# Optimization experiments

Hardware: AMD Instinct MI355X
Metric: run time of the kernel (lower is better)

The kernel has to match this reference:

```python
import jax, jax.numpy as jnp
import numpy as np
from jax import lax

V, D, L, H, MAXLEN = 32000, 512, 6, 8, 1024
DH = D // H
DFF = 4 * D
B, T = 8, 1024


def _ln(x, g, b, eps=1e-5):
    m = jnp.mean(x, axis=-1, keepdims=True)
    v = jnp.var(x, axis=-1, keepdims=True)
    return (x - m) * lax.rsqrt(v + eps) * g + b


def setup_inputs() -> dict:
    key = jax.random.key(0)
    ks = jax.random.split(key, 16)
    s = 0.02
    inp = {
        "idx": jax.random.randint(ks[0], (B, T), 0, V, dtype=jnp.int32),
        "wte": jax.random.normal(ks[1], (V, D), jnp.float32) * s,   # tied with head
        "wpe": jax.random.normal(ks[2], (MAXLEN, D), jnp.float32) * s,
        # per-layer stacked params [L, ...]
        "ln1_g": jnp.ones((L, D), jnp.float32),
        "ln1_b": jnp.zeros((L, D), jnp.float32),
        "w_qkv": jax.random.normal(ks[3], (L, D, 3 * D), jnp.float32) * s,
        "b_qkv": jnp.zeros((L, 3 * D), jnp.float32),
        "w_ao": jax.random.normal(ks[4], (L, D, D), jnp.float32) * s,
        "b_ao": jnp.zeros((L, D), jnp.float32),
        "ln2_g": jnp.ones((L, D), jnp.float32),
        "ln2_b": jnp.zeros((L, D), jnp.float32),
        "w_fc": jax.random.normal(ks[5], (L, D, DFF), jnp.float32) * s,
        "b_fc": jnp.zeros((L, DFF), jnp.float32),
        "w_pr": jax.random.normal(ks[6], (L, DFF, D), jnp.float32) * s,
        "b_pr": jnp.zeros((L, D), jnp.float32),
        "lnf_g": jnp.ones((D,), jnp.float32),
        "lnf_b": jnp.zeros((D,), jnp.float32),
    }
    return inp


def reference(idx, wte, wpe, ln1_g, ln1_b, w_qkv, b_qkv, w_ao, b_ao,
              ln2_g, ln2_b, w_fc, b_fc, w_pr, b_pr, lnf_g, lnf_b):
    Bx, Tx = idx.shape
    x = wte[idx] + wpe[:Tx]                      # [B,T,D]
    causal = jnp.tril(jnp.ones((Tx, Tx), bool))  # [T,T]
    scale = 1.0 / np.sqrt(DH)

    def block(x, p):
        (g1, b1, wqkv, bqkv, wao, bao, g2, b2, wfc, bfc, wpr, bpr) = p
        h = _ln(x, g1, b1)
        qkv = h @ wqkv + bqkv                    # [B,T,3D]
        q, k, v = jnp.split(qkv, 3, axis=-1)
        q = q.reshape(Bx, Tx, H, DH)
        k = k.reshape(Bx, Tx, H, DH)
        v = v.reshape(Bx, Tx, H, DH)
        att = jnp.einsum('bqhd,bkhd->bhqk', q, k) * scale
        att = jnp.where(causal, att, -jnp.inf)
        att = jax.nn.softmax(att, axis=-1)
        y = jnp.einsum('bhqk,bkhd->bqhd', att, v).reshape(Bx, Tx, D)
        x = x + y @ wao + bao
        h = _ln(x, g2, b2)
        h = jax.nn.gelu(h @ wfc + bfc, approximate=False)
        x = x + h @ wpr + bpr
        return x, None

    params = (ln1_g, ln1_b, w_qkv, b_qkv, w_ao, b_ao,
              ln2_g, ln2_b, w_fc, b_fc, w_pr, b_pr)
    x, _ = lax.scan(block, x, params)
    x = _ln(x, lnf_g, lnf_b)
    logits = x @ wte.T                           # tied head, [B,T,V]
    return logits
```

## Files before the change

### kernel.cpp

```cpp
#include <hip/hip_runtime.h>
#include <hip/hip_bf16.h>
#include <math.h>

#define V_   32000
#define D_   512
#define L_   6
#define H_   8
#define DH_  64
#define DFF_ 2048
#define B_   8
#define T_   1024
#define BT_  (B_*T_)

typedef __attribute__((ext_vector_type(4))) float f32x4;
typedef __attribute__((ext_vector_type(8))) short short8;
using bf16_t = __hip_bfloat16;

__device__ __forceinline__ float b2f(unsigned short u) {
    union { unsigned int i; float f; } v; v.i = ((unsigned int)u) << 16; return v.f;
}
__device__ __forceinline__ unsigned short f2b(float f) {
    bf16_t h = __float2bfloat16(f);
    return *reinterpret_cast<unsigned short*>(&h);
}
__device__ __forceinline__ void gl16(const void* g, void* l) {
    __builtin_amdgcn_global_load_lds((const __attribute__((address_space(1))) void*)g,
                                     (__attribute__((address_space(3))) void*)l, 16, 0, 0);
}
__device__ __forceinline__ float gelu_exact(float v) {
    return 0.5f * v * (1.0f + erff(v * 0.70710678118654752f));
}

__global__ __launch_bounds__(128) void embed_ln_kernel(
        const int* __restrict__ idx, const float* __restrict__ wte,
        const float* __restrict__ wpe, const float* __restrict__ g,
        const float* __restrict__ bb, float* __restrict__ x,
        bf16_t* __restrict__ hout) {
    int bt = blockIdx.x;
    int tt = bt & (T_ - 1);
    int tok = idx[bt];
    int i = threadIdx.x;
    float4 a = ((const float4*)(wte + (size_t)tok * D_))[i];
    float4 p = ((const float4*)(wpe + (size_t)tt * D_))[i];
    float4 v = make_float4(a.x + p.x, a.y + p.y, a.z + p.z, a.w + p.w);
    ((float4*)(x + (size_t)bt * D_))[i] = v;

    float s  = v.x + v.y + v.z + v.w;
    float sq = v.x*v.x + v.y*v.y + v.z*v.z + v.w*v.w;
    #pragma unroll
    for (int o = 32; o > 0; o >>= 1) {
        s  += __shfl_down(s,  o);
        sq += __shfl_down(sq, o);
    }
    __shared__ float ss[2], ssq[2];
    if ((i & 63) == 0) { ss[i >> 6] = s; ssq[i >> 6] = sq; }
    __syncthreads();
    float mean = (ss[0] + ss[1]) * (1.0f / D_);
    float var  = (ssq[0] + ssq[1]) * (1.0f / D_) - mean * mean;
    float rstd = rsqrtf(var + 1e-5f);
    float4 gg = ((const float4*)g)[i];
    float4 b2 = ((const float4*)bb)[i];
    ushort4 o4;
    o4.x = f2b((v.x - mean) * rstd * gg.x + b2.x);
    o4.y = f2b((v.y - mean) * rstd * gg.y + b2.y);
    o4.z = f2b((v.z - mean) * rstd * gg.z + b2.z);
    o4.w = f2b((v.w - mean) * rstd * gg.w + b2.w);
    ((ushort4*)(hout + (size_t)bt * D_))[i] = o4;
}

__global__ __launch_bounds__(128) void ln_kernel(
        const float* __restrict__ x, const float* __restrict__ g,
        const float* __restrict__ b, bf16_t* __restrict__ out) {
    int bt = blockIdx.x;
    int i  = threadIdx.x;
    float4 v = ((const float4*)(x + (size_t)bt * D_))[i];
    float s  = v.x + v.y + v.z + v.w;
    float sq = v.x*v.x + v.y*v.y + v.z*v.z + v.w*v.w;
    #pragma unroll
    for (int o = 32; o > 0; o >>= 1) {
        s  += __shfl_down(s,  o);
        sq += __shfl_down(sq, o);
    }
    __shared__ float ss[2], ssq[2];
    if ((i & 63) == 0) { ss[i >> 6] = s; ssq[i >> 6] = sq; }
    __syncthreads();
    float mean = (ss[0] + ss[1]) * (1.0f / D_);
    float var  = (ssq[0] + ssq[1]) * (1.0f / D_) - mean * mean;
    float rstd = rsqrtf(var + 1e-5f);
    float4 gg = ((const float4*)g)[i];
    float4 bb = ((const float4*)b)[i];
    ushort4 o4;
    o4.x = f2b((v.x - mean) * rstd * gg.x + bb.x);
    o4.y = f2b((v.y - mean) * rstd * gg.y + bb.y);
    o4.z = f2b((v.z - mean) * rstd * gg.z + bb.z);
    o4.w = f2b((v.w - mean) * rstd * gg.w + bb.w);
    ((ushort4*)(out + (size_t)bt * D_))[i] = o4;
}

__global__ __launch_bounds__(256) void conv_kernel(
        const float* __restrict__ s, bf16_t* __restrict__ d, int n4) {
    int i = blockIdx.x * 256 + threadIdx.x;
    if (i >= n4) return;
    float4 f = ((const float4*)s)[i];
    ushort4 u = make_ushort4(f2b(f.x), f2b(f.y), f2b(f.z), f2b(f.w));
    ((ushort4*)d)[i] = u;
}

__global__ __launch_bounds__(256) void tconv_kernel(
        const float* __restrict__ src, bf16_t* __restrict__ dst, int K, int N) {
    size_t ls = (size_t)K * N;
    const float* s = src + blockIdx.z * ls;
    bf16_t* d = dst + blockIdx.z * ls;
    __shared__ float tile[32][33];
    int n0 = blockIdx.x * 32, k0 = blockIdx.y * 32;
    int c = threadIdx.x & 31, r8 = threadIdx.x >> 5;
    #pragma unroll
    for (int i = 0; i < 4; ++i) {
        int r = r8 + i * 8;
        tile[r][c] = s[(size_t)(k0 + r) * N + n0 + c];
    }
    __syncthreads();
    #pragma unroll
    for (int i = 0; i < 4; ++i) {
        int r = r8 + i * 8;
        d[(size_t)(n0 + r) * K + k0 + c] = __float2bfloat16(tile[c][r]);
    }
}

template<int BK, int ACT, bool OBF, bool RES, bool CONVB>
__global__ __launch_bounds__(256) void mm_kernel(
        const bf16_t* __restrict__ A,
        const bf16_t* __restrict__ Bt,
        const float*  __restrict__ Bf,
        const float*  __restrict__ bias,
        const float*  __restrict__ res,
        void* __restrict__ Cout,
        int M, int N, int K)
{
    constexpr int SLOTS = BK / 8;
    constexpr int CH    = BK / 16;
    __shared__ __align__(16) unsigned short As[128 * BK];
    __shared__ __align__(16) unsigned short Bs[128 * BK];
    const int nwg = gridDim.x;
    const int orig = blockIdx.x;
    const int q8 = nwg >> 3, r8 = nwg & 7;
    const int xcd = orig & 7, lin = orig >> 3;
    const int wg = (xcd < r8) ? xcd * (q8 + 1) + lin
                              : r8 * (q8 + 1) + (xcd - r8) * q8 + lin;
    const int gym = M >> 7;
    const int by = wg % gym;
    const int bx = wg / gym;

    const int t    = threadIdx.x;
    const int row0 = by * 128;
    const int col0 = bx * 128;
    const int lane = t & 63;
    const int wid  = t >> 6;
    const int wm   = (wid & 1) * 64;
    const int wn   = (wid >> 1) * 64;
    const int fr   = lane & 15;
    const int fq   = lane >> 4;

    f32x4 acc[4][4];
    #pragma unroll
    for (int m = 0; m < 4; ++m)
        #pragma unroll
        for (int n = 0; n < 4; ++n)
            acc[m][n] = (f32x4)(0.0f);

    const unsigned short* Ab  = (const unsigned short*)A;
    const unsigned short* Btb = (const unsigned short*)Bt;

    for (int k0 = 0; k0 < K; k0 += BK) {
        __syncthreads();
        #pragma unroll
        for (int i = 0; i < CH; ++i) {
            int c = t + i * 256;
            int row = c / SLOTS;
            int sl  = (c & (SLOTS - 1)) ^ (row & 7);
            gl16(Ab + (size_t)(row0 + row) * K + k0 + sl * 8, As + (size_t)c * 8);
        }
        if (!CONVB) {
            #pragma unroll
            for (int i = 0; i < CH; ++i) {
                int c = t + i * 256;
                int row = c / SLOTS;
                int sl  = (c & (SLOTS - 1)) ^ (row & 7);
                gl16(Btb + (size_t)(col0 + row) * K + k0 + sl * 8, Bs + (size_t)c * 8);
            }
        } else {
            #pragma unroll
            for (int i = 0; i < CH; ++i) {
                int c = t + i * 256;
                int row = c / SLOTS;
                int sl  = (c & (SLOTS - 1)) ^ (row & 7);
                const float* sp = Bf + (size_t)(col0 + row) * K + k0 + sl * 8;
                float4 f0 = ((const float4*)sp)[0];
                float4 f1 = ((const float4*)sp)[1];
                short8 pk;
                pk[0] = f2b(f0.x); pk[1] = f2b(f0.y); pk[2] = f2b(f0.z); pk[3] = f2b(f0.w);
                pk[4] = f2b(f1.x); pk[5] = f2b(f1.y); pk[6] = f2b(f1.z); pk[7] = f2b(f1.w);
                *(short8*)(Bs + (size_t)c * 8) = pk;
            }
        }
        __syncthreads();

        #pragma unroll
        for (int kk = 0; kk < BK / 32; ++kk) {
            short8 av[4], bv[4];
            #pragma unroll
            for (int m = 0; m < 4; ++m) {
                int R = wm + m * 16 + fr;
                int sl = (kk * 4 + fq) ^ (fr & 7);
                av[m] = *(const short8*)(As + (size_t)R * BK + sl * 8);
            }
            #pragma unroll
            for (int n = 0; n < 4; ++n) {
                int R = wn + n * 16 + fr;
                int sl = (kk * 4 + fq) ^ (fr & 7);
                bv[n] = *(const short8*)(Bs + (size_t)R * BK + sl * 8);
            }
            #pragma unroll
            for (int m = 0; m < 4; ++m)
                #pragma unroll
                for (int n = 0; n < 4; ++n)
                    acc[m][n] = __builtin_amdgcn_mfma_f32_16x16x32_bf16(av[m], bv[n], acc[m][n], 0, 0, 0);
        }
    }

    #pragma unroll
    for (int n = 0; n < 4; ++n) {
        int col = col0 + wn + n * 16 + fr;
        float bb = bias ? bias[col] : 0.0f;
        #pragma unroll
        for (int m = 0; m < 4; ++m) {
            int rbase = row0 + wm + m * 16 + fq * 4;
            #pragma unroll
            for (int r = 0; r < 4; ++r) {
                float v = acc[m][n][r] + bb;
                if (ACT == 1) v = gelu_exact(v);
                size_t off = (size_t)(rbase + r) * N + col;
                if (RES) v += res[off];
                if (OBF) ((bf16_t*)Cout)[off] = __float2bfloat16(v);
                else     ((float*)Cout)[off]  = v;
            }
        }
    }
}

#define MM8_PHASE(MH, NH, HALF, SRCB, R0, DSTB)                               \
  {                                                                           \
    short8 af[2][4]; short8 bg[2][2];                                         \
    _Pragma("unroll")                                                         \
    for (int ks = 0; ks < 2; ++ks) {                                          \
      _Pragma("unroll")                                                       \
      for (int m = 0; m < 4; ++m) {                                           \
        int row = ((MH)*4 + m)*32 + wm*16 + fr;                               \
        int sl  = (ks*4 + fq) ^ (fr & 7);                                     \
        af[ks][m] = *(const short8*)(curA + (size_t)row*64 + (size_t)sl*8);   \
      }                                                                       \
      _Pragma("unroll")                                                       \
      for (int n = 0; n < 2; ++n) {                                           \
        int col = ((NH)*2 + n)*64 + wn*16 + fr;                               \
        int sl  = (ks*4 + fq) ^ (fr & 7);                                     \
        bg[ks][n] = *(const short8*)(curB + (size_t)col*64 + (size_t)sl*8);   \
      }                                                                       \
    }                                                                         \
    if (pf) {                                                                 \
      _Pragma("unroll")                                                       \
      for (int i = 0; i < 2; ++i) {                                           \
        int c = (HALF)*1024 + i*512 + t;                                      \
        int row = c >> 3, sl = (c & 7) ^ (row & 7);                           \
        gl16(SRCB + (size_t)((R0) + row)*K + k0n + sl*8,                      \
             DSTB + (size_t)c*8);                                             \
      }                                                                       \
      asm volatile("s_waitcnt vmcnt(2)" ::: "memory");                        \
    } else if ((MH) == 0 && (NH) == 0) {                                      \
      asm volatile("s_waitcnt vmcnt(0)" ::: "memory");                        \
    }                                                                         \
    asm volatile("s_barrier" ::: "memory");                                   \
    asm volatile("s_waitcnt lgkmcnt(0)" ::: "memory");                        \
    __builtin_amdgcn_sched_barrier(0);                                        \
    __builtin_amdgcn_s_setprio(1);                                            \
    _Pragma("unroll")                                                         \
    for (int ks = 0; ks < 2; ++ks)                                            \
      _Pragma("unroll")                                                       \
      for (int m = 0; m < 4; ++m)                                             \
        _Pragma("unroll")                                                     \
        for (int n = 0; n < 2; ++n)                                           \
          acc[(MH)*4+m][(NH)*2+n] = __builtin_amdgcn_mfma_f32_16x16x32_bf16(  \
              af[ks][m], bg[ks][n], acc[(MH)*4+m][(NH)*2+n], 0, 0, 0);        \
    __builtin_amdgcn_s_setprio(0);                                            \
    __builtin_amdgcn_sched_barrier(0);                                        \
    asm volatile("s_barrier" ::: "memory");                                   \
  }

template<int ACT, bool OBF>
__global__ __launch_bounds__(512) void mm8_kernel(
        const bf16_t* __restrict__ A,
        const bf16_t* __restrict__ Bt,
        const float*  __restrict__ bias,
        void* __restrict__ Cout,
        int M, int N, int K)
{
    __shared__ __align__(16) unsigned short sA[2][256 * 64];
    __shared__ __align__(16) unsigned short sB[2][256 * 64];

    const int nwg = gridDim.x;
    const int orig = blockIdx.x;
    const int q8 = nwg >> 3, r8 = nwg & 7;
    const int xcd = orig & 7, lin = orig >> 3;
    const int wg = (xcd < r8) ? xcd * (q8 + 1) + lin
                              : r8 * (q8 + 1) + (xcd - r8) * q8 + lin;
    const int gym = M >> 8;
    const int by = wg % gym;
    const int bx = wg / gym;
    const int row0 = by * 256;
    const int col0 = bx * 256;

    const int t    = threadIdx.x;
    const int lane = t & 63;
    const int wid  = t >> 6;
    const int wm   = wid >> 2;
    const int wn   = wid & 3;
    const int fr   = lane & 15;
    const int fq   = lane >> 4;

    const unsigned short* Ab = (const unsigned short*)A;
    const unsigned short* Bb = (const unsigned short*)Bt;

    f32x4 acc[8][4];
    #pragma unroll
    for (int m = 0; m < 8; ++m)
        #pragma unroll
        for (int n = 0; n < 4; ++n)
            acc[m][n] = (f32x4)(0.0f);

    const int NK = K >> 6;

    #pragma unroll
    for (int h = 0; h < 2; ++h)
        #pragma unroll
        for (int i = 0; i < 2; ++i) {
            int c = h * 1024 + i * 512 + t;
            int row = c >> 3, sl = (c & 7) ^ (row & 7);
            gl16(Ab + (size_t)(row0 + row) * K + sl * 8, &sA[0][(size_t)c * 8]);
            gl16(Bb + (size_t)(col0 + row) * K + sl * 8, &sB[0][(size_t)c * 8]);
        }
    asm volatile("s_waitcnt vmcnt(0)" ::: "memory");
    asm volatile("s_barrier" ::: "memory");

    for (int s = 0; s < NK; ++s) {
        const unsigned short* curA = sA[s & 1];
        const unsigned short* curB = sB[s & 1];
        unsigned short* nxA = (unsigned short*)sA[(s + 1) & 1];
        unsigned short* nxB = (unsigned short*)sB[(s + 1) & 1];
        const int k0n = (s + 1) << 6;
        const bool pf = (s + 1) < NK;
        MM8_PHASE(0, 0, 0, Ab, row0, nxA)
        MM8_PHASE(1, 0, 0, Bb, col0, nxB)
        MM8_PHASE(0, 1, 1, Ab, row0, nxA)
        MM8_PHASE(1, 1, 1, Bb, col0, nxB)
    }

    #pragma unroll
    for (int n = 0; n < 4; ++n) {
        int col = col0 + n * 64 + wn * 16 + fr;
        float bb = bias ? bias[col] : 0.0f;
        #pragma unroll
        for (int m = 0; m < 8; ++m) {
            int rbase = row0 + m * 32 + wm * 16 + fq * 4;
            #pragma unroll
            for (int r = 0; r < 4; ++r) {
                float v = acc[m][n][r] + bb;
                if (ACT == 1) v = gelu_exact(v);
                size_t off = (size_t)(rbase + r) * N + col;
                if (OBF) ((bf16_t*)Cout)[off] = __float2bfloat16(v);
                else     ((float*)Cout)[off]  = v;
            }
        }
    }
}

__global__ __launch_bounds__(512, 2) void flash_kernel(
        const bf16_t* __restrict__ qkv, bf16_t* __restrict__ y)
{
    __shared__ __align__(16) unsigned short Ks[2][64][72];
    __shared__ __align__(16) unsigned short Vt[2][64][72];
    __shared__ __align__(16) unsigned short Pls[128][72];

    const int qt = (T_ / 128 - 1) - (blockIdx.x >> 6);
    const int bh = blockIdx.x & 63;
    const int h  = bh & (H_ - 1);
    const int b  = bh >> 3;
    const int t  = threadIdx.x;
    const int lane = t & 63;
    const int w    = t >> 6;
    const int fr   = lane & 15;
    const int fq   = lane >> 4;
    const int sj   = t >> 3;
    const int sseg = t & 7;

    const unsigned short* qkvb = (const unsigned short*)qkv;

    short8 avq[2];
    {
        const unsigned short* qrow = qkvb +
            (size_t)(b * T_ + qt * 128 + w * 16 + fr) * (3 * D_) + h * DH_;
        avq[0] = *(const short8*)(qrow + fq * 8);
        avq[1] = *(const short8*)(qrow + 32 + fq * 8);
    }

    float mi[4], li[4];
    f32x4 oacc[4];
    #pragma unroll
    for (int r = 0; r < 4; ++r) { mi[r] = -INFINITY; li[r] = 0.0f; }
    #pragma unroll
    for (int d = 0; d < 4; ++d) oacc[d] = (f32x4)(0.0f);

    const int nt = 2 * qt + 2;

    short8 kreg, vreg;
    {
        const unsigned short* kr = qkvb +
            (size_t)(b * T_ + sj) * (3 * D_) + D_ + h * DH_ + sseg * 8;
        kreg = *(const short8*)kr;
        vreg = *(const short8*)(kr + D_);
    }
    *(short8*)&Ks[0][sj][sseg * 8] = kreg;
    {
        int dbase = sseg * 8;
        Vt[0][dbase + 0][sj] = vreg[0]; Vt[0][dbase + 1][sj] = vreg[1];
        Vt[0][dbase + 2][sj] = vreg[2]; Vt[0][dbase + 3][sj] = vreg[3];
        Vt[0][dbase + 4][sj] = vreg[4]; Vt[0][dbase + 5][sj] = vreg[5];
        Vt[0][dbase + 6][sj] = vreg[6]; Vt[0][dbase + 7][sj] = vreg[7];
    }
    __syncthreads();

    for (int jt = 0; jt < nt; ++jt) {
        const int cur = jt & 1;
        const bool pf = (jt + 1) < nt;
        if (pf) {
            const unsigned short* kr = qkvb +
                (size_t)(b * T_ + (jt + 1) * 64 + sj) * (3 * D_) + D_ + h * DH_ + sseg * 8;
            kreg = *(const short8*)kr;
            vreg = *(const short8*)(kr + D_);
        }

        f32x4 s[4];
        #pragma unroll
        for (int jb = 0; jb < 4; ++jb) s[jb] = (f32x4)(0.0f);
        #pragma unroll
        for (int ks = 0; ks < 2; ++ks) {
            #pragma unroll
            for (int jb = 0; jb < 4; ++jb) {
                short8 bv = *(const short8*)(&Ks[cur][jb * 16 + fr][ks * 32 + fq * 8]);
                s[jb] = __builtin_amdgcn_mfma_f32_16x16x32_bf16(avq[ks], bv, s[jb], 0, 0, 0);
            }
        }

        float sv[4][4];
        const int qgb = qt * 128 + w * 16 + fq * 4;
        #pragma unroll
        for (int jb = 0; jb < 4; ++jb) {
            int jg = jt * 64 + jb * 16 + fr;
            #pragma unroll
            for (int r = 0; r < 4; ++r) {
                float x = s[jb][r] * 0.125f;
                sv[jb][r] = (jg > qgb + r) ? -INFINITY : x;
            }
        }

        #pragma unroll
        for (int r = 0; r < 4; ++r) {
            float tm = fmaxf(fmaxf(sv[0][r], sv[1][r]), fmaxf(sv[2][r], sv[3][r]));
            tm = fmaxf(tm, __shfl_xor(tm, 1));
            tm = fmaxf(tm, __shfl_xor(tm, 2));
            tm = fmaxf(tm, __shfl_xor(tm, 4));
            tm = fmaxf(tm, __shfl_xor(tm, 8));
            float mnew = fmaxf(mi[r], tm);
            float corr = __expf(mi[r] - mnew);
            float tsum = 0.0f;
            #pragma unroll
            for (int jb = 0; jb < 4; ++jb) {
                float p = __expf(sv[jb][r] - mnew);
                sv[jb][r] = p;
                tsum += p;
            }
            tsum += __shfl_xor(tsum, 1);
            tsum += __shfl_xor(tsum, 2);
            tsum += __shfl_xor(tsum, 4);
            tsum += __shfl_xor(tsum, 8);
            li[r] = li[r] * corr + tsum;
            mi[r] = mnew;
            #pragma unroll
            for (int db = 0; db < 4; ++db) oacc[db][r] *= corr;
        }

        #pragma unroll
        for (int jb = 0; jb < 4; ++jb)
            #pragma unroll
            for (int r = 0; r < 4; ++r)
                Pls[w * 16 + fq * 4 + r][jb * 16 + fr] = f2b(sv[jb][r]);

        #pragma unroll
        for (int ks = 0; ks < 2; ++ks) {
            short8 ap = *(const short8*)(&Pls[w * 16 + fr][ks * 32 + fq * 8]);
            #pragma unroll
            for (int db = 0; db < 4; ++db) {
                short8 bv = *(const short8*)(&Vt[cur][db * 16 + fr][ks * 32 + fq * 8]);
                oacc[db] = __builtin_amdgcn_mfma_f32_16x16x32_bf16(ap, bv, oacc[db], 0, 0, 0);
            }
        }

        __syncthreads();
        if (pf) {
            *(short8*)&Ks[cur ^ 1][sj][sseg * 8] = kreg;
            int dbase = sseg * 8;
            Vt[cur ^ 1][dbase + 0][sj] = vreg[0]; Vt[cur ^ 1][dbase + 1][sj] = vreg[1];
            Vt[cur ^ 1][dbase + 2][sj] = vreg[2]; Vt[cur ^ 1][dbase + 3][sj] = vreg[3];
            Vt[cur ^ 1][dbase + 4][sj] = vreg[4]; Vt[cur ^ 1][dbase + 5][sj] = vreg[5];
            Vt[cur ^ 1][dbase + 6][sj] = vreg[6]; Vt[cur ^ 1][dbase + 7][sj] = vreg[7];
        }
        __syncthreads();
    }

    unsigned short* yb = (unsigned short*)y;
    #pragma unroll
    for (int r = 0; r < 4; ++r) {
        float inv = 1.0f / li[r];
        size_t row = (size_t)(b * T_ + qt * 128 + w * 16 + fq * 4 + r);
        #pragma unroll
        for (int db = 0; db < 4; ++db)
            yb[row * D_ + h * DH_ + db * 16 + fr] = f2b(oacc[db][r] * inv);
    }
}

extern "C" void kernel_launch(void* const* d_in, const int* in_sizes, int n_in,
                              void* d_out, int out_size, void* d_ws, size_t ws_size,
                              hipStream_t stream) {
    const int*   idx   = (const int*)  d_in[0];
    const float* wte   = (const float*)d_in[1];
    const float* wpe   = (const float*)d_in[2];
    const float* ln1_g = (const float*)d_in[3];
    const float* ln1_b = (const float*)d_in[4];
    const float* w_qkv = (const float*)d_in[5];
    const float* b_qkv = (const float*)d_in[6];
    const float* w_ao  = (const float*)d_in[7];
    const float* b_ao  = (const float*)d_in[8];
    const float* ln2_g = (const float*)d_in[9];
    const float* ln2_b = (const float*)d_in[10];
    const float* w_fc  = (const float*)d_in[11];
    const float* b_fc  = (const float*)d_in[12];
    const float* w_pr  = (const float*)d_in[13];
    const float* b_pr  = (const float*)d_in[14];
    const float* lnf_g = (const float*)d_in[15];
    const float* lnf_b = (const float*)d_in[16];
    float* outf = (float*)d_out;

    char* base = (char*)d_out;
    size_t off = 0;
    auto alloc = [&](size_t bytes) {
        void* p = base + off;
        off += (bytes + 255) & ~(size_t)255;
        return p;
    };
    bf16_t* wqkvT = (bf16_t*)alloc((size_t)L_ * 3 * D_ * D_ * 2);
    bf16_t* waoT  = (bf16_t*)alloc((size_t)L_ * D_ * D_ * 2);
    bf16_t* wfcT  = (bf16_t*)alloc((size_t)L_ * DFF_ * D_ * 2);
    bf16_t* wprT  = (bf16_t*)alloc((size_t)L_ * D_ * DFF_ * 2);
    bf16_t* qkvb  = (bf16_t*)alloc((size_t)BT_ * 3 * D_ * 2);
    bf16_t* yb    = (bf16_t*)alloc((size_t)BT_ * D_ * 2);
    bf16_t* hab   = (bf16_t*)alloc((size_t)BT_ * D_ * 2);
    bf16_t* fcb   = (bf16_t*)alloc((size_t)BT_ * DFF_ * 2);
    float*  xb    = (float*) alloc((size_t)BT_ * D_ * 4);

    bf16_t* hfin = (bf16_t*)d_ws;
    size_t hbytes = ((size_t)BT_ * D_ * 2 + 255) & ~(size_t)255;
    bool wte_ws = ws_size >= hbytes + (size_t)V_ * D_ * 2 + 256;
    bf16_t* wteb = wte_ws ? (bf16_t*)((char*)d_ws + hbytes) : nullptr;

    if (wte_ws)
        conv_kernel<<<(V_ * D_ / 4 + 255) / 256, 256, 0, stream>>>(wte, wteb, V_ * D_ / 4);
    tconv_kernel<<<dim3(3 * D_ / 32, D_ / 32, L_), 256, 0, stream>>>(w_qkv, wqkvT, D_, 3 * D_);
    tconv_kernel<<<dim3(D_ / 32, D_ / 32, L_), 256, 0, stream>>>(w_ao, waoT, D_, D_);
    tconv_kernel<<<dim3(DFF_ / 32, D_ / 32, L_), 256, 0, stream>>>(w_fc, wfcT, D_, DFF_);
    tconv_kernel<<<dim3(D_ / 32, DFF_ / 32, L_), 256, 0, stream>>>(w_pr, wprT, DFF_, D_);

    embed_ln_kernel<<<BT_, 128, 0, stream>>>(idx, wte, wpe, ln1_g, ln1_b, xb, hab);

    for (int l = 0; l < L_; ++l) {
        mm8_kernel<0, true><<<(BT_ / 256) * (3 * D_ / 256), 512, 0, stream>>>(
            hab, wqkvT + (size_t)l * 3 * D_ * D_, b_qkv + (size_t)l * 3 * D_,
            qkvb, BT_, 3 * D_, D_);
        flash_kernel<<<512, 512, 0, stream>>>(qkvb, yb);
        mm_kernel<128, 0, false, true, false><<<4 * 64, 256, 0, stream>>>(
            yb, waoT + (size_t)l * D_ * D_, nullptr, b_ao + (size_t)l * D_,
            xb, xb, BT_, D_, D_);
        ln_kernel<<<BT_, 128, 0, stream>>>(xb, ln2_g + (size_t)l * D_, ln2_b + (size_t)l * D_, hab);
        mm8_kernel<1, true><<<(BT_ / 256) * (DFF_ / 256), 512, 0, stream>>>(
            hab, wfcT + (size_t)l * DFF_ * D_, b_fc + (size_t)l * DFF_,
            fcb, BT_, DFF_, D_);
        mm_kernel<128, 0, false, true, false><<<4 * 64, 256, 0, stream>>>(
            fcb, wprT + (size_t)l * D_ * DFF_, nullptr, b_pr + (size_t)l * D_,
            xb, xb, BT_, D_, DFF_);
        if (l < L_ - 1)
            ln_kernel<<<BT_, 128, 0, stream>>>(xb, ln1_g + (size_t)(l + 1) * D_,
                                               ln1_b + (size_t)(l + 1) * D_, hab);
        else
            ln_kernel<<<BT_, 128, 0, stream>>>(xb, lnf_g, lnf_b, hfin);
    }

    if (wte_ws)
        mm8_kernel<0, false><<<(BT_ / 256) * (V_ / 256), 512, 0, stream>>>(
            hfin, wteb, nullptr, outf, BT_, V_, D_);
    else
        mm_kernel<64, 0, false, false, true><<<250 * 64, 256, 0, stream>>>(
            hfin, nullptr, wte, nullptr, nullptr, outf, BT_, V_, D_);
}
```

Baseline: 1.688 ms.

## Fuse residual projections with LayerNorm and pre-transpose V for flash attention

Adds an mm_ln_kernel that computes the output projection GEMM over full rows (32 rows by 512 columns per block), adds bias and residual, and applies LayerNorm in the epilogue. It replaces both residual GEMMs and their separate ln_kernel passes, removing a full read and write of the activations per LN. Flash attention now reads V from a buffer pre-transposed by a new vtrans kernel and loads K/V tiles with direct global-to-LDS swizzled loads, dropping the scalar transpose writes and one barrier per iteration. In exchange the fused GEMM launches only 256 blocks with a large LDS footprint, which may underuse the GPU, and the V transpose adds an extra pass.

New measurement: 1.686 ms. No clear change (-0.1%).

```diff
diff --git a/kernel.cpp b/kernel.cpp
--- a/kernel.cpp
+++ b/kernel.cpp
@@ -68,35 +68,6 @@
     ((ushort4*)(hout + (size_t)bt * D_))[i] = o4;
 }
 
-__global__ __launch_bounds__(128) void ln_kernel(
-        const float* __restrict__ x, const float* __restrict__ g,
-        const float* __restrict__ b, bf16_t* __restrict__ out) {
-    int bt = blockIdx.x;
-    int i  = threadIdx.x;
-    float4 v = ((const float4*)(x + (size_t)bt * D_))[i];
-    float s  = v.x + v.y + v.z + v.w;
-    float sq = v.x*v.x + v.y*v.y + v.z*v.z + v.w*v.w;
-    #pragma unroll
-    for (int o = 32; o > 0; o >>= 1) {
-        s  += __shfl_down(s,  o);
-        sq += __shfl_down(sq, o);
-    }
-    __shared__ float ss[2], ssq[2];
-    if ((i & 63) == 0) { ss[i >> 6] = s; ssq[i >> 6] = sq; }
-    __syncthreads();
-    float mean = (ss[0] + ss[1]) * (1.0f / D_);
-    float var  = (ssq[0] + ssq[1]) * (1.0f / D_) - mean * mean;
-    float rstd = rsqrtf(var + 1e-5f);
-    float4 gg = ((const float4*)g)[i];
-    float4 bb = ((const float4*)b)[i];
-    ushort4 o4;
-    o4.x = f2b((v.x - mean) * rstd * gg.x + bb.x);
-    o4.y = f2b((v.y - mean) * rstd * gg.y + bb.y);
-    o4.z = f2b((v.z - mean) * rstd * gg.z + bb.z);
-    o4.w = f2b((v.w - mean) * rstd * gg.w + bb.w);
-    ((ushort4*)(out + (size_t)bt * D_))[i] = o4;
-}
-
 __global__ __launch_bounds__(256) void conv_kernel(
         const float* __restrict__ s, bf16_t* __restrict__ d, int n4) {
     int i = blockIdx.x * 256 + threadIdx.x;
@@ -124,6 +95,28 @@
     for (int i = 0; i < 4; ++i) {
         int r = r8 + i * 8;
         d[(size_t)(n0 + r) * K + k0 + c] = __float2bfloat16(tile[c][r]);
+    }
+}
+
+__global__ __launch_bounds__(256) void vtrans_kernel(
+        const bf16_t* __restrict__ qkv, bf16_t* __restrict__ vt) {
+    const unsigned short* q = (const unsigned short*)qkv;
+    unsigned short* d = (unsigned short*)vt;
+    __shared__ unsigned short tile[32][33];
+    int bh = blockIdx.z;
+    int b  = bh >> 3, h = bh & 7;
+    int t0 = blockIdx.x * 32, d0 = blockIdx.y * 32;
+    int c = threadIdx.x & 31, r8 = threadIdx.x >> 5;
+    #pragma unroll
+    for (int i = 0; i < 4; ++i) {
+        int r = r8 + i * 8;
+        tile[r][c] = q[(size_t)(b * T_ + t0 + r) * (3 * D_) + 2 * D_ + h * DH_ + d0 + c];
+    }
+    __syncthreads();
+    #pragma unroll
+    for (int i = 0; i < 4; ++i) {
+        int r = r8 + i * 8;
+        d[(size_t)(bh * DH_ + d0 + r) * T_ + t0 + c] = tile[c][r];
     }
 }
 
@@ -243,6 +236,120 @@
                 if (RES) v += res[off];
                 if (OBF) ((bf16_t*)Cout)[off] = __float2bfloat16(v);
                 else     ((float*)Cout)[off]  = v;
+            }
+        }
+    }
+}
+
+__global__ __launch_bounds__(512) void mm_ln_kernel(
+        const bf16_t* __restrict__ A,
+        const bf16_t* __restrict__ Bt,
+        const float*  __restrict__ bias,
+        float*        __restrict__ xio,
+        const float*  __restrict__ g,
+        const float*  __restrict__ lb,
+        bf16_t*       __restrict__ hout,
+        int M, int K)
+{
+    __shared__ __align__(16) unsigned short As[32 * 64];
+    __shared__ __align__(16) unsigned short Bs[512 * 64];
+    __shared__ float stats[32][8][2];
+
+    const int row0 = blockIdx.x * 32;
+    const int t    = threadIdx.x;
+    const int lane = t & 63;
+    const int w    = t >> 6;
+    const int fr   = lane & 15;
+    const int fq   = lane >> 4;
+
+    const unsigned short* Ab  = (const unsigned short*)A;
+    const unsigned short* Btb = (const unsigned short*)Bt;
+
+    f32x4 acc[2][4];
+    #pragma unroll
+    for (int m = 0; m < 2; ++m)
+        #pragma unroll
+        for (int n = 0; n < 4; ++n)
+            acc[m][n] = (f32x4)(0.0f);
+
+    for (int k0 = 0; k0 < K; k0 += 64) {
+        __syncthreads();
+        if (t < 256) {
+            int c = t;
+            int row = c >> 3, sl = (c & 7) ^ (row & 7);
+            gl16(Ab + (size_t)(row0 + row) * K + k0 + sl * 8, As + (size_t)c * 8);
+        }
+        #pragma unroll
+        for (int i = 0; i < 8; ++i) {
+            int c = t + i * 512;
+            int row = c >> 3, sl = (c & 7) ^ (row & 7);
+            gl16(Btb + (size_t)row * K + k0 + sl * 8, Bs + (size_t)c * 8);
+        }
+        __syncthreads();
+
+        #pragma unroll
+        for (int kk = 0; kk < 2; ++kk) {
+            int sl = (kk * 4 + fq) ^ (fr & 7);
+            short8 av[2], bv[4];
+            #pragma unroll
+            for (int m = 0; m < 2; ++m)
+                av[m] = *(const short8*)(As + (size_t)(m * 16 + fr) * 64 + sl * 8);
+            #pragma unroll
+            for (int n = 0; n < 4; ++n)
+                bv[n] = *(const short8*)(Bs + (size_t)(w * 64 + n * 16 + fr) * 64 + sl * 8);
+            #pragma unroll
+            for (int m = 0; m < 2; ++m)
+                #pragma unroll
+                for (int n = 0; n < 4; ++n)
+                    acc[m][n] = __builtin_amdgcn_mfma_f32_16x16x32_bf16(av[m], bv[n], acc[m][n], 0, 0, 0);
+        }
+    }
+
+    float vv[2][4][4];
+    #pragma unroll
+    for (int m = 0; m < 2; ++m) {
+        #pragma unroll
+        for (int r = 0; r < 4; ++r) {
+            int rowl = m * 16 + fq * 4 + r;
+            float ps = 0.0f, pq = 0.0f;
+            #pragma unroll
+            for (int n = 0; n < 4; ++n) {
+                int col = w * 64 + n * 16 + fr;
+                float v = acc[m][n][r] + bias[col] +
+                          xio[(size_t)(row0 + rowl) * D_ + col];
+                vv[m][n][r] = v;
+                ps += v; pq += v * v;
+            }
+            ps += __shfl_xor(ps, 1); pq += __shfl_xor(pq, 1);
+            ps += __shfl_xor(ps, 2); pq += __shfl_xor(pq, 2);
+            ps += __shfl_xor(ps, 4); pq += __shfl_xor(pq, 4);
+            ps += __shfl_xor(ps, 8); pq += __shfl_xor(pq, 8);
+            if (fr == 0) { stats[rowl][w][0] = ps; stats[rowl][w][1] = pq; }
+        }
+    }
+    __syncthreads();
+
+    #pragma unroll
+    for (int m = 0; m < 2; ++m) {
+        #pragma unroll
+        for (int r = 0; r < 4; ++r) {
+            int rowl = m * 16 + fq * 4 + r;
+            float su = 0.0f, sq = 0.0f;
+            #pragma unroll
+            for (int ww = 0; ww < 8; ++ww) {
+                su += stats[rowl][ww][0];
+                sq += stats[rowl][ww][1];
+            }
+            float mean = su * (1.0f / D_);
+            float var  = sq * (1.0f / D_) - mean * mean;
+            float rstd = rsqrtf(var + 1e-5f);
+            #pragma unroll
+            for (int n = 0; n < 4; ++n) {
+                int col = w * 64 + n * 16 + fr;
+                float v = vv[m][n][r];
+                size_t off = (size_t)(row0 + rowl) * D_ + col;
+                xio[off] = v;
+                hout[off] = __float2bfloat16((v - mean) * rstd * g[col] + lb[col]);
             }
         }
     }
@@ -382,11 +489,12 @@
     }
 }
 
-__global__ __launch_bounds__(512, 2) void flash_kernel(
-        const bf16_t* __restrict__ qkv, bf16_t* __restrict__ y)
+__global__ __launch_bounds__(512, 6) void flash_kernel(
+        const bf16_t* __restrict__ qkv, const bf16_t* __restrict__ vt,
+        bf16_t* __restrict__ y)
 {
-    __shared__ __align__(16) unsigned short Ks[2][64][72];
-    __shared__ __align__(16) unsigned short Vt[2][64][72];
+    __shared__ __align__(16) unsigned short Ks[2][64 * 64];
+    __shared__ __align__(16) unsigned short Vs[2][64 * 64];
     __shared__ __align__(16) unsigned short Pls[128][72];
 
     const int qt = (T_ / 128 - 1) - (blockIdx.x >> 6);
@@ -398,10 +506,11 @@
     const int w    = t >> 6;
     const int fr   = lane & 15;
     const int fq   = lane >> 4;
-    const int sj   = t >> 3;
-    const int sseg = t & 7;
+    const int srow = t >> 3;
+    const int ssl  = (t & 7) ^ (srow & 7);
 
     const unsigned short* qkvb = (const unsigned short*)qkv;
+    const unsigned short* vtb  = (const unsigned short*)vt;
 
     short8 avq[2];
     {
@@ -420,31 +529,20 @@
 
     const int nt = 2 * qt + 2;
 
-    short8 kreg, vreg;
-    {
-        const unsigned short* kr = qkvb +
-            (size_t)(b * T_ + sj) * (3 * D_) + D_ + h * DH_ + sseg * 8;
-        kreg = *(const short8*)kr;
-        vreg = *(const short8*)(kr + D_);
-    }
-    *(short8*)&Ks[0][sj][sseg * 8] = kreg;
-    {
-        int dbase = sseg * 8;
-        Vt[0][dbase + 0][sj] = vreg[0]; Vt[0][dbase + 1][sj] = vreg[1];
-        Vt[0][dbase + 2][sj] = vreg[2]; Vt[0][dbase + 3][sj] = vreg[3];
-        Vt[0][dbase + 4][sj] = vreg[4]; Vt[0][dbase + 5][sj] = vreg[5];
-        Vt[0][dbase + 6][sj] = vreg[6]; Vt[0][dbase + 7][sj] = vreg[7];
-    }
+    gl16(qkvb + (size_t)(b * T_ + srow) * (3 * D_) + D_ + h * DH_ + ssl * 8,
+         &Ks[0][(size_t)t * 8]);
+    gl16(vtb + (size_t)(bh * DH_ + srow) * T_ + ssl * 8,
+         &Vs[0][(size_t)t * 8]);
     __syncthreads();
 
     for (int jt = 0; jt < nt; ++jt) {
         const int cur = jt & 1;
-        const bool pf = (jt + 1) < nt;
-        if (pf) {
-            const unsigned short* kr = qkvb +
-                (size_t)(b * T_ + (jt + 1) * 64 + sj) * (3 * D_) + D_ + h * DH_ + sseg * 8;
-            kreg = *(const short8*)kr;
-            vreg = *(const short8*)(kr + D_);
+        if (jt + 1 < nt) {
+            gl16(qkvb + (size_t)(b * T_ + (jt + 1) * 64 + srow) * (3 * D_)
+                     + D_ + h * DH_ + ssl * 8,
+                 &Ks[cur ^ 1][(size_t)t * 8]);
+            gl16(vtb + (size_t)(bh * DH_ + srow) * T_ + (jt + 1) * 64 + ssl * 8,
+                 &Vs[cur ^ 1][(size_t)t * 8]);
         }
 
         f32x4 s[4];
@@ -452,9 +550,10 @@
         for (int jb = 0; jb < 4; ++jb) s[jb] = (f32x4)(0.0f);
         #pragma unroll
         for (int ks = 0; ks < 2; ++ks) {
+            int sl = (ks * 4 + fq) ^ (fr & 7);
             #pragma unroll
             for (int jb = 0; jb < 4; ++jb) {
-                short8 bv = *(const short8*)(&Ks[cur][jb * 16 + fr][ks * 32 + fq * 8]);
+                short8 bv = *(const short8*)(&Ks[cur][(size_t)(jb * 16 + fr) * 64 + sl * 8]);
                 s[jb] = __builtin_amdgcn_mfma_f32_16x16x32_bf16(avq[ks], bv, s[jb], 0, 0, 0);
             }
         }
@@ -506,22 +605,14 @@
         #pragma unroll
         for (int ks = 0; ks < 2; ++ks) {
             short8 ap = *(const short8*)(&Pls[w * 16 + fr][ks * 32 + fq * 8]);
+            int sl = (ks * 4 + fq) ^ (fr & 7);
             #pragma unroll
             for (int db = 0; db < 4; ++db) {
-                short8 bv = *(const short8*)(&Vt[cur][db * 16 + fr][ks * 32 + fq * 8]);
+                short8 bv = *(const short8*)(&Vs[cur][(size_t)(db * 16 + fr) * 64 + sl * 8]);
                 oacc[db] = __builtin_amdgcn_mfma_f32_16x16x32_bf16(ap, bv, oacc[db], 0, 0, 0);
             }
         }
 
-        __syncthreads();
-        if (pf) {
-            *(short8*)&Ks[cur ^ 1][sj][sseg * 8] = kreg;
-            int dbase = sseg * 8;
-            Vt[cur ^ 1][dbase + 0][sj] = vreg[0]; Vt[cur ^ 1][dbase + 1][sj] = vreg[1];
-            Vt[cur ^ 1][dbase + 2][sj] = vreg[2]; Vt[cur ^ 1][dbase + 3][sj] = vreg[3];
-            Vt[cur ^ 1][dbase + 4][sj] = vreg[4]; Vt[cur ^ 1][dbase + 5][sj] = vreg[5];
-            Vt[cur ^ 1][dbase + 6][sj] = vreg[6]; Vt[cur ^ 1][dbase + 7][sj] = vreg[7];
-        }
         __syncthreads();
     }
 
@@ -570,6 +661,7 @@
     bf16_t* wfcT  = (bf16_t*)alloc((size_t)L_ * DFF_ * D_ * 2);
     bf16_t* wprT  = (bf16_t*)alloc((size_t)L_ * D_ * DFF_ * 2);
     bf16_t* qkvb  = (bf16_t*)alloc((size_t)BT_ * 3 * D_ * 2);
+    bf16_t* vtbuf = (bf16_t*)alloc((size_t)B_ * H_ * DH_ * T_ * 2);
     bf16_t* yb    = (bf16_t*)alloc((size_t)BT_ * D_ * 2);
     bf16_t* hab   = (bf16_t*)alloc((size_t)BT_ * D_ * 2);
     bf16_t* fcb   = (bf16_t*)alloc((size_t)BT_ * DFF_ * 2);
@@ -593,22 +685,23 @@
         mm8_kernel<0, true><<<(BT_ / 256) * (3 * D_ / 256), 512, 0, stream>>>(
             hab, wqkvT + (size_t)l * 3 * D_ * D_, b_qkv + (size_t)l * 3 * D_,
             qkvb, BT_, 3 * D_, D_);
-        flash_kernel<<<512, 512, 0, stream>>>(qkvb, yb);
-        mm_kernel<128, 0, false, true, false><<<4 * 64, 256, 0, stream>>>(
-            yb, waoT + (size_t)l * D_ * D_, nullptr, b_ao + (size_t)l * D_,
-            xb, xb, BT_, D_, D_);
-        ln_kernel<<<BT_, 128, 0, stream>>>(xb, ln2_g + (size_t)l * D_, ln2_b + (size_t)l * D_, hab);
+        vtrans_kernel<<<dim3(T_ / 32, DH_ / 32, B_ * H_), 256, 0, stream>>>(qkvb, vtbuf);
+        flash_kernel<<<512, 512, 0, stream>>>(qkvb, vtbuf, yb);
+        mm_ln_kernel<<<BT_ / 32, 512, 0, stream>>>(
+            yb, waoT + (size_t)l * D_ * D_, b_ao + (size_t)l * D_,
+            xb, ln2_g + (size_t)l * D_, ln2_b + (size_t)l * D_, hab, BT_, D_);
         mm8_kernel<1, true><<<(BT_ / 256) * (DFF_ / 256), 512, 0, stream>>>(
             hab, wfcT + (size_t)l * DFF_ * D_, b_fc + (size_t)l * DFF_,
             fcb, BT_, DFF_, D_);
-        mm_kernel<128, 0, false, true, false><<<4 * 64, 256, 0, stream>>>(
-            fcb, wprT + (size_t)l * D_ * DFF_, nullptr, b_pr + (size_t)l * D_,
-            xb, xb, BT_, D_, DFF_);
         if (l < L_ - 1)
-            ln_kernel<<<BT_, 128, 0, stream>>>(xb, ln1_g + (size_t)(l + 1) * D_,
-                                               ln1_b + (size_t)(l + 1) * D_, hab);
+            mm_ln_kernel<<<BT_ / 32, 512, 0, stream>>>(
+                fcb, wprT + (size_t)l * D_ * DFF_, b_pr + (size_t)l * D_,
+                xb, ln1_g + (size_t)(l + 1) * D_, ln1_b + (size_t)(l + 1) * D_,
+                hab, BT_, DFF_);
         else
-            ln_kernel<<<BT_, 128, 0, stream>>>(xb, lnf_g, lnf_b, hfin);
+            mm_ln_kernel<<<BT_ / 32, 512, 0, stream>>>(
+                fcb, wprT + (size_t)l * D_ * DFF_, b_pr + (size_t)l * D_,
+                xb, lnf_g, lnf_b, hfin, BT_, DFF_);
     }
 
     if (wte_ws)
```
